# Kernel optimization log

Measured on AMD Instinct MI355X. Metric: run time of the kernel, lower is better.

Reference implementation:

```python
import jax, jax.numpy as jnp
import numpy as np

B, N, H = 256, 512, 128          # batch of subgraphs, max elements per subgraph, hidden size
NH, DEPTH = 2, 3                 # num_attention_heads (hardcoded 2 in SubGraph), depth
DH = H // NH                     # per-head dim
EPS = 1e-5
NEG = -10000.0


def setup_inputs() -> dict:
    key = jax.random.key(0)
    ks = jax.random.split(key, 12)
    s = 0.02
    x = jax.random.normal(ks[0], (B, N, H), jnp.float32)
    lengths = jax.random.randint(ks[1], (B,), 1, N + 1, jnp.int32)
    # MLP layer_0: Linear + LayerNorm + ReLU
    W0 = jax.random.normal(ks[2], (H, H), jnp.float32) * s
    b0 = jnp.zeros((H,), jnp.float32)
    g0 = jnp.ones((H,), jnp.float32)
    be0 = jnp.zeros((H,), jnp.float32)
    # MLP layer_0_again
    W1 = jax.random.normal(ks[3], (H, H), jnp.float32) * s
    b1 = jnp.zeros((H,), jnp.float32)
    g1 = jnp.ones((H,), jnp.float32)
    be1 = jnp.zeros((H,), jnp.float32)
    # GlobalGraph q/k/v per depth (no output projection in VectorNet GlobalGraph)
    Wq = jax.random.normal(ks[4], (DEPTH, H, H), jnp.float32) * s
    bq = jnp.zeros((DEPTH, H), jnp.float32)
    Wk = jax.random.normal(ks[5], (DEPTH, H, H), jnp.float32) * s
    bk = jnp.zeros((DEPTH, H), jnp.float32)
    Wv = jax.random.normal(ks[6], (DEPTH, H, H), jnp.float32) * s
    bv = jnp.zeros((DEPTH, H), jnp.float32)
    # post-block LayerNorms (layers_2)
    gl = jnp.ones((DEPTH, H), jnp.float32)
    bl = jnp.zeros((DEPTH, H), jnp.float32)
    return dict(hidden_states=x, lengths=lengths, W0=W0, b0=b0, g0=g0, be0=be0,
                W1=W1, b1=b1, g1=g1, be1=be1, Wq=Wq, bq=bq, Wk=Wk, bk=bk,
                Wv=Wv, bv=bv, gl=gl, bl=bl)


def _layer_norm(x, g, b):
    m = jnp.mean(x, axis=-1, keepdims=True)
    v = jnp.mean((x - m) ** 2, axis=-1, keepdims=True)
    return (x - m) * jax.lax.rsqrt(v + EPS) * g + b


def _mlp(x, W, b, g, be):
    return jax.nn.relu(_layer_norm(x @ W + b, g, be))


def reference(hidden_states, lengths, W0, b0, g0, be0, W1, b1, g1, be1,
              Wq, bq, Wk, bk, Wv, bv, gl, bl):
    # vectorized variable-length square mask: mask[i, :len, :len] = 1
    valid = (jnp.arange(N) < lengths[:, None])                      # [B, N] bool
    attn_mask = (valid[:, :, None] & valid[:, None, :]).astype(hidden_states.dtype)  # [B, N, N]
    bias = (1.0 - attn_mask)[:, None, :, :] * NEG                   # [B, 1, N, N]

    h = _mlp(hidden_states, W0, b0, g0, be0)
    h = _mlp(h, W1, b1, g1, be1)

    scale = 1.0 / np.sqrt(DH)
    for d in range(DEPTH):  # small fixed structural loop
        temp = h
        q = (h @ Wq[d] + bq[d]).reshape(B, N, NH, DH)
        k = (h @ Wk[d] + bk[d]).reshape(B, N, NH, DH)
        v = (h @ Wv[d] + bv[d]).reshape(B, N, NH, DH)
        scores = jnp.einsum('bnhd,bmhd->bhnm', q, k) * scale + bias  # [B, NH, N, N]
        probs = jax.nn.softmax(scores, axis=-1)
        ctx = jnp.einsum('bhnm,bmhd->bnhd', probs, v).reshape(B, N, H)
        h = _layer_norm(jax.nn.relu(ctx) + temp, gl[d], bl[d])
    return jnp.max(h, axis=1)  # [B, H]
```

## Files before the change

### kernel.cpp

```cpp
#include <hip/hip_runtime.h>
#include <hip/hip_bf16.h>

#define BB 256
#define NN 512
#define HH 128
#define MM (BB*NN)

typedef unsigned short u16;
typedef unsigned int   u32;
typedef __attribute__((ext_vector_type(8))) short bf16x8;
typedef __attribute__((ext_vector_type(4))) float f32x4;
typedef __attribute__((ext_vector_type(16))) float f32x16;

#define LOG2E  1.4426950408889634f
#define QSCALE (0.125f * LOG2E)
#define NEGB   (-10000.0f * LOG2E)

__device__ __forceinline__ int kswz(int row, int cbyte) {
  return row*128 + (cbyte ^ ((row & 7) << 4));
}
__device__ __forceinline__ int wswz(int row, int cbyte) {
  return row*256 + (cbyte ^ ((row & 7) << 4));
}

__device__ __forceinline__ u16 f2bf(float x) {
  __hip_bfloat16 h = __float2bfloat16(x);
  return *reinterpret_cast<u16*>(&h);
}
__device__ __forceinline__ float bf2f(u16 x) {
  return __uint_as_float(((u32)x) << 16);
}

__device__ __forceinline__ void gld_lds16(const void* g, void* l) {
  __builtin_amdgcn_global_load_lds(
      (__attribute__((address_space(1))) const unsigned int*)g,
      (__attribute__((address_space(3))) unsigned int*)l, 16, 0, 0);
}

__global__ __launch_bounds__(256) void wt_prep(
    const float* __restrict__ W0, const float* __restrict__ W1,
    const float* __restrict__ Wq, const float* __restrict__ Wk,
    const float* __restrict__ Wv, u16* __restrict__ wt)
{
  __shared__ u16 tile[128*128];
  const int t = threadIdx.x;
  const int i = blockIdx.x;
  const float* src;
  if (i == 0) src = W0;
  else if (i == 1) src = W1;
  else {
    const int d = (i-2)/3, which = (i-2)%3;
    src = (which==0 ? Wq : which==1 ? Wk : Wv) + d*HH*HH;
  }
  u16* dst = wt + (size_t)i*HH*HH;

  #pragma unroll
  for (int j = 0; j < 8; j++) {
    const int chunk = t + 256*j;
    const int k = chunk >> 4, c8 = (chunk & 15)*8;
    const float4 a = *(const float4*)&src[k*HH + c8];
    const float4 b = *(const float4*)&src[k*HH + c8 + 4];
    union { u16 s[8]; uint4 v; } u;
    u.s[0]=f2bf(a.x); u.s[1]=f2bf(a.y); u.s[2]=f2bf(a.z); u.s[3]=f2bf(a.w);
    u.s[4]=f2bf(b.x); u.s[5]=f2bf(b.y); u.s[6]=f2bf(b.z); u.s[7]=f2bf(b.w);
    *(uint4*)&tile[k*128 + (((chunk & 15) ^ ((k>>3)&7)) << 3)] = u.v;
  }
  __syncthreads();
  #pragma unroll
  for (int j = 0; j < 8; j++) {
    const int chunk = t + 256*j;
    const int c = chunk >> 4, kb8 = (chunk & 15)*8;
    union { u16 s[8]; uint4 v; } u;
    #pragma unroll
    for (int e = 0; e < 8; e++) {
      const int k = kb8 + e;
      u.s[e] = tile[k*128 + ((((c>>3) ^ ((k>>3)&7)) << 3) | (c & 7))];
    }
    *(uint4*)&dst[c*HH + kb8] = u.v;
  }
}

template<bool F32IN, bool LNRELU>
__device__ __forceinline__ void linear_body(
    const void* __restrict__ Xv, const u16* __restrict__ WT,
    const float* __restrict__ bias, const float* __restrict__ gamma,
    const float* __restrict__ beta, u16* __restrict__ OUT,
    u16* wt_s, u16* xs)
{
  const int t = threadIdx.x;
  const int lane = t & 63, w = t >> 6;
  const int l4 = lane >> 4, l15 = lane & 15;
  const long row0 = (long)blockIdx.x * 128;

  {
    const int rr = lane >> 4;
    const int cb = (lane & 15) * 16;
    #pragma unroll
    for (int i = 0; i < 8; i++) {
      const int seg = w*8 + i;
      const int row = seg*4 + rr;
      gld_lds16((const char*)WT + (size_t)row*256 + (cb ^ ((row & 7) << 4)),
                (char*)wt_s + seg*1024);
    }
    if constexpr (!F32IN) {
      const char* xp = (const char*)((const u16*)Xv + row0*HH);
      #pragma unroll
      for (int i = 0; i < 8; i++) {
        const int seg = w*8 + i;
        const int row = seg*4 + rr;
        gld_lds16(xp + (size_t)row*256 + (cb ^ ((row & 7) << 4)),
                  (char*)xs + seg*1024);
      }
    }
  }
  if constexpr (F32IN) {
    const float* xp = (const float*)Xv + row0*HH;
    #pragma unroll
    for (int i = 0; i < 8; i++) {
      const int chunk = t + 256*i;
      const int r = chunk >> 4, c8 = (chunk & 15)*8;
      const float4 a = *(const float4*)&xp[r*HH + c8];
      const float4 b = *(const float4*)&xp[r*HH + c8 + 4];
      union { u16 s[8]; uint4 v; } u;
      u.s[0]=f2bf(a.x); u.s[1]=f2bf(a.y); u.s[2]=f2bf(a.z); u.s[3]=f2bf(a.w);
      u.s[4]=f2bf(b.x); u.s[5]=f2bf(b.y); u.s[6]=f2bf(b.z); u.s[7]=f2bf(b.w);
      *(uint4*)((char*)xs + wswz(r, c8*2)) = u.v;
    }
  }
  __syncthreads();

  f32x4 acc[2][8];
  #pragma unroll
  for (int m = 0; m < 2; m++)
    #pragma unroll
    for (int n = 0; n < 8; n++)
      { acc[m][n][0]=0.f; acc[m][n][1]=0.f; acc[m][n][2]=0.f; acc[m][n][3]=0.f; }

  #pragma unroll
  for (int ks = 0; ks < 4; ks++) {
    bf16x8 af[2], bf[8];
    #pragma unroll
    for (int m = 0; m < 2; m++)
      af[m] = *(const bf16x8*)((const char*)xs + wswz(w*32 + m*16 + l15, ks*64 + l4*16));
    #pragma unroll
    for (int n = 0; n < 8; n++)
      bf[n] = *(const bf16x8*)((const char*)wt_s + wswz(n*16 + l15, ks*64 + l4*16));
    #pragma unroll
    for (int m = 0; m < 2; m++)
      #pragma unroll
      for (int n = 0; n < 8; n++)
        acc[m][n] = __builtin_amdgcn_mfma_f32_16x16x32_bf16(af[m], bf[n], acc[m][n], 0, 0, 0);
  }

  float bia[8], gam[8], bet[8];
  #pragma unroll
  for (int n = 0; n < 8; n++) {
    bia[n] = bias[n*16 + l15];
    if constexpr (LNRELU) { gam[n] = gamma[n*16 + l15]; bet[n] = beta[n*16 + l15]; }
  }
  #pragma unroll
  for (int m = 0; m < 2; m++) {
    #pragma unroll
    for (int r = 0; r < 4; r++) {
      const long row = row0 + w*32 + m*16 + l4*4 + r;
      float v[8];
      #pragma unroll
      for (int n = 0; n < 8; n++) v[n] = acc[m][n][r] + bia[n];
      if constexpr (LNRELU) {
        float s = 0.f, ss = 0.f;
        #pragma unroll
        for (int n = 0; n < 8; n++) { s += v[n]; ss += v[n]*v[n]; }
        #pragma unroll
        for (int off = 1; off < 16; off <<= 1) {
          s  += __shfl_xor(s,  off);
          ss += __shfl_xor(ss, off);
        }
        const float mean = s * (1.0f/128.0f);
        const float rstd = rsqrtf(ss*(1.0f/128.0f) - mean*mean + 1e-5f);
        #pragma unroll
        for (int n = 0; n < 8; n++)
          v[n] = fmaxf((v[n] - mean)*rstd*gam[n] + bet[n], 0.0f);
      }
      u16* op = OUT + row*HH + l15;
      #pragma unroll
      for (int n = 0; n < 8; n++) op[n*16] = f2bf(v[n]);
    }
  }
}

template<bool F32IN, bool LNRELU>
__global__ __launch_bounds__(256) void linear_mfma(
    const void* __restrict__ Xv, const u16* __restrict__ WT,
    const float* __restrict__ bias, const float* __restrict__ gamma,
    const float* __restrict__ beta, u16* __restrict__ OUT)
{
  __shared__ u16 wt_s[128*128];
  __shared__ u16 xs[128*128];
  linear_body<F32IN, LNRELU>(Xv, WT, bias, gamma, beta, OUT, wt_s, xs);
}

__global__ __launch_bounds__(256) void qkv_mfma(
    const u16* __restrict__ X, const u16* __restrict__ WTd,
    const float* __restrict__ bq, const float* __restrict__ bk,
    const float* __restrict__ bv,
    u16* __restrict__ qb, u16* __restrict__ kb, u16* __restrict__ vb)
{
  __shared__ u16 wt_s[128*128];
  __shared__ u16 xs[128*128];
  const int y = blockIdx.y;
  const u16* WT = WTd + y*HH*HH;
  const float* bias = (y==0) ? bq : (y==1) ? bk : bv;
  u16* OUT = (y==0) ? qb : (y==1) ? kb : vb;
  linear_body<false, false>(X, WT, bias, nullptr, nullptr, OUT, wt_s, xs);
}

__global__ __launch_bounds__(256) void transpose_v_kernel(
    const u16* __restrict__ vb, u16* __restrict__ vT)
{
  __shared__ u16 tile[128*128];
  const int t  = threadIdx.x;
  const int b  = blockIdx.x >> 2;
  const int n0 = (blockIdx.x & 3) * 128;

  #pragma unroll
  for (int i = 0; i < 8; i++) {
    const int chunk = t + 256*i;
    const int n = chunk >> 4, cslot = chunk & 15;
    uint4 d = *(const uint4*)(vb + ((size_t)(b*NN + n0 + n))*HH + cslot*8);
    *(uint4*)&tile[n*128 + ((cslot ^ ((n>>3)&7)) << 3)] = d;
  }
  __syncthreads();
  #pragma unroll
  for (int i = 0; i < 8; i++) {
    const int chunk = t + 256*i;
    const int c = chunk >> 4, nb = (chunk & 15) * 8;
    union { u16 s[8]; uint4 v; } u;
    #pragma unroll
    for (int j = 0; j < 8; j++) {
      const int n = nb + j;
      u.s[j] = tile[n*128 + ((((c>>3) ^ ((n>>3)&7)) << 3) | (c & 7))];
    }
    u16* op = vT + (((size_t)(b*2 + (c>>6)))*64 + (c & 63))*NN + n0 + nb;
    *(uint4*)op = u.v;
  }
}

__global__ __launch_bounds__(256) void attn_kernel(
    const u16* __restrict__ Q, const u16* __restrict__ K,
    const u16* __restrict__ VT, const int* __restrict__ lengths,
    u16* __restrict__ CTX)
{
  __shared__ u16 sh_q[128*64];
  __shared__ u16 sh_k[2][64*64];
  __shared__ u16 sh_v[2][64*64];
  const int t    = threadIdx.x;
  const int lane = t & 63;
  const int w    = t >> 6;
  const int bid  = blockIdx.x;
  const int qt   = bid & 3;
  const int head = (bid >> 2) & 1;
  const int b    = bid >> 3;
  const int L    = lengths[b];
  const int q0   = qt * 128;
  const int l31  = lane & 31;
  const int hi   = lane >> 5;
  const int rr8  = lane >> 3;
  const int cb8  = (lane & 7) * 16;

  const char* qbase  = (const char*)(Q + ((size_t)(b*NN + q0))*HH + head*64);
  const char* kbase0 = (const char*)(K + ((size_t)(b*NN))*HH + head*64);
  const char* vbase0 = (const char*)(VT + (((size_t)(b*2 + head))*64)*NN);

  #pragma unroll
  for (int i = 0; i < 4; i++) {
    const int seg = w*4 + i;
    const int row = seg*8 + rr8;
    gld_lds16(qbase + (size_t)row*256 + (cb8 ^ ((row&7)<<4)),
              (char*)sh_q + seg*1024);
  }
  #pragma unroll
  for (int i = 0; i < 2; i++) {
    const int seg = w*2 + i;
    const int row = seg*8 + rr8;
    const int sw = cb8 ^ ((row&7)<<4);
    gld_lds16(kbase0 + (size_t)row*256  + sw, (char*)sh_k[0] + seg*1024);
    gld_lds16(vbase0 + (size_t)row*1024 + sw, (char*)sh_v[0] + seg*1024);
  }
  __syncthreads();

  bf16x8 qf[4];
  #pragma unroll
  for (int st = 0; st < 4; st++)
    qf[st] = *(const bf16x8*)((const char*)sh_q + kswz(w*32 + l31, st*32 + hi*16));

  f32x16 cacc[2];
  #pragma unroll
  for (int r = 0; r < 16; r++) { cacc[0][r] = 0.f; cacc[1][r] = 0.f; }
  float l_run = 0.0f;

  const bool q_allv   = (q0 + w*32 + 31) < L;
  const bool q_allinv = (q0 + w*32) >= L;
  const bool qv       = (q0 + w*32 + l31) < L;
  const int  nch      = (q0 + 127 < L) ? ((L + 63) >> 6) : 8;

  for (int ch = 0; ch < nch; ch++) {
    const int cur = ch & 1;
    if (ch + 1 < nch) {
      const char* kb_ = kbase0 + (size_t)(ch+1)*64*256;
      const char* vb_ = vbase0 + (size_t)(ch+1)*128;
      #pragma unroll
      for (int i = 0; i < 2; i++) {
        const int seg = w*2 + i;
        const int row = seg*8 + rr8;
        const int sw = cb8 ^ ((row&7)<<4);
        gld_lds16(kb_ + (size_t)row*256  + sw, (char*)sh_k[cur^1] + seg*1024);
        gld_lds16(vb_ + (size_t)row*1024 + sw, (char*)sh_v[cur^1] + seg*1024);
      }
    }

    const bool skip = q_allv && (ch*64 >= L);
    if (!skip) {
      f32x16 sacc[2];
      #pragma unroll
      for (int r = 0; r < 16; r++) { sacc[0][r] = 0.f; sacc[1][r] = 0.f; }
      #pragma unroll
      for (int st = 0; st < 4; st++) {
        const bf16x8 kf0 = *(const bf16x8*)((const char*)sh_k[cur] + kswz(l31,      st*32 + hi*16));
        const bf16x8 kf1 = *(const bf16x8*)((const char*)sh_k[cur] + kswz(32 + l31, st*32 + hi*16));
        sacc[0] = __builtin_amdgcn_mfma_f32_32x32x16_bf16(kf0, qf[st], sacc[0], 0, 0, 0);
        sacc[1] = __builtin_amdgcn_mfma_f32_32x32x16_bf16(kf1, qf[st], sacc[1], 0, 0, 0);
      }

      const bool fast = (ch*64 + 63 < L) || q_allinv;
      u32 pw[2][8];
      #pragma unroll
      for (int kb2 = 0; kb2 < 2; kb2++) {
        float p[16];
        float psum = 0.f;
        if (fast) {
          #pragma unroll
          for (int r = 0; r < 16; r++) {
            p[r] = exp2f(sacc[kb2][r] * QSCALE);
            psum += p[r];
          }
        } else {
          #pragma unroll
          for (int r = 0; r < 16; r++) {
            const int key = ch*64 + kb2*32 + (r&3) + 8*(r>>2) + 4*hi;
            const float bias = (qv && key >= L) ? NEGB : 0.0f;
            p[r] = exp2f(fmaf(sacc[kb2][r], QSCALE, bias));
            psum += p[r];
          }
        }
        l_run += psum;
        #pragma unroll
        for (int mm = 0; mm < 4; mm++)
          #pragma unroll
          for (int e = 0; e < 2; e++)
            pw[kb2][mm*2+e] = (u32)f2bf(p[4*mm+2*e]) | ((u32)f2bf(p[4*mm+2*e+1]) << 16);
      }

      #pragma unroll
      for (int kb2 = 0; kb2 < 2; kb2++) {
        #pragma unroll
        for (int st = 0; st < 2; st++) {
          const u32 w00 = pw[kb2][(2*st+0)*2+0], w01 = pw[kb2][(2*st+0)*2+1];
          const u32 w10 = pw[kb2][(2*st+1)*2+0], w11 = pw[kb2][(2*st+1)*2+1];
          const u32 own0 = hi ? w10 : w00;
          const u32 own1 = hi ? w11 : w01;
          const u32 snd0 = hi ? w00 : w10;
          const u32 snd1 = hi ? w01 : w11;
          const u32 rcv0 = (u32)__shfl_xor((int)snd0, 32);
          const u32 rcv1 = (u32)__shfl_xor((int)snd1, 32);
          union { u32 u[4]; bf16x8 v; } pb;
          pb.u[0] = hi ? rcv0 : own0;
          pb.u[1] = hi ? rcv1 : own1;
          pb.u[2] = hi ? own0 : rcv0;
          pb.u[3] = hi ? own1 : rcv1;
          #pragma unroll
          for (int db = 0; db < 2; db++) {
            const bf16x8 vf = *(const bf16x8*)((const char*)sh_v[cur] +
                                kswz(db*32 + l31, kb2*64 + st*32 + hi*16));
            cacc[db] = __builtin_amdgcn_mfma_f32_32x32x16_bf16(vf, pb.v, cacc[db], 0, 0, 0);
          }
        }
      }
    }

    __syncthreads();
  }

  const float l_full = l_run + __shfl_xor(l_run, 32);
  const float inv = 1.0f / l_full;
  const int qrow = q0 + w*32 + l31;
  u16* crow = CTX + ((size_t)(b*NN) + qrow)*HH + head*64;
  #pragma unroll
  for (int db = 0; db < 2; db++)
    #pragma unroll
    for (int mm = 0; mm < 4; mm++) {
      const int dh0 = db*32 + mm*8 + hi*4;
      uint2 o;
      o.x = (u32)f2bf(cacc[db][4*mm+0]*inv) | ((u32)f2bf(cacc[db][4*mm+1]*inv) << 16);
      o.y = (u32)f2bf(cacc[db][4*mm+2]*inv) | ((u32)f2bf(cacc[db][4*mm+3]*inv) << 16);
      *(uint2*)(crow + dh0) = o;
    }
}

__global__ __launch_bounds__(256) void resln_kernel(
    const u16* __restrict__ CTX, u16* Hb,
    const float* __restrict__ gl, const float* __restrict__ bl)
{
  const int t = threadIdx.x;
  const int lane = t & 63;
  const long row = (long)blockIdx.x*4 + (t >> 6);
  const u32 craw = *(const u32*)&CTX[row*HH + lane*2];
  const u32 hraw = *(const u32*)&Hb[row*HH + lane*2];
  const float c0 = bf2f((u16)(craw & 0xffff)), c1 = bf2f((u16)(craw >> 16));
  const float h0 = bf2f((u16)(hraw & 0xffff)), h1 = bf2f((u16)(hraw >> 16));
  const float x0 = fmaxf(c0, 0.0f) + h0;
  const float x1 = fmaxf(c1, 0.0f) + h1;
  float s = x0 + x1, ss = x0*x0 + x1*x1;
  #pragma unroll
  for (int off = 1; off < 64; off <<= 1) {
    s  += __shfl_xor(s,  off);
    ss += __shfl_xor(ss, off);
  }
  const float mean = s * (1.0f/128.0f);
  const float rstd = rsqrtf(ss*(1.0f/128.0f) - mean*mean + 1e-5f);
  const float o0 = (x0 - mean)*rstd*gl[lane*2]   + bl[lane*2];
  const float o1 = (x1 - mean)*rstd*gl[lane*2+1] + bl[lane*2+1];
  *(u32*)&Hb[row*HH + lane*2] = (u32)f2bf(o0) | ((u32)f2bf(o1) << 16);
}

__global__ __launch_bounds__(256) void maxred_kernel(
    const u16* __restrict__ Hb, float* __restrict__ out)
{
  __shared__ float red[256];
  const int b = blockIdx.x;
  const int col = threadIdx.x & 127, half = threadIdx.x >> 7;
  const u16* hp = Hb + ((size_t)b*NN + half*256)*HH + col;
  float m0 = -3.0e38f, m1 = -3.0e38f, m2 = -3.0e38f, m3 = -3.0e38f;
  for (int r = 0; r < 256; r += 4) {
    m0 = fmaxf(m0, bf2f(hp[(r+0)*HH]));
    m1 = fmaxf(m1, bf2f(hp[(r+1)*HH]));
    m2 = fmaxf(m2, bf2f(hp[(r+2)*HH]));
    m3 = fmaxf(m3, bf2f(hp[(r+3)*HH]));
  }
  red[threadIdx.x] = fmaxf(fmaxf(m0, m1), fmaxf(m2, m3));
  __syncthreads();
  if (half == 0) out[(size_t)b*HH + col] = fmaxf(red[col], red[col + 128]);
}

extern "C" void kernel_launch(void* const* d_in, const int* in_sizes, int n_in,
                              void* d_out, int out_size, void* d_ws, size_t ws_size,
                              hipStream_t stream)
{
  const float* x   = (const float*)d_in[0];
  const int* lens  = (const int*)d_in[1];
  const float* W0  = (const float*)d_in[2];
  const float* b0  = (const float*)d_in[3];
  const float* g0  = (const float*)d_in[4];
  const float* be0 = (const float*)d_in[5];
  const float* W1  = (const float*)d_in[6];
  const float* b1  = (const float*)d_in[7];
  const float* g1  = (const float*)d_in[8];
  const float* be1 = (const float*)d_in[9];
  const float* Wq  = (const float*)d_in[10];
  const float* bq  = (const float*)d_in[11];
  const float* Wk  = (const float*)d_in[12];
  const float* bk  = (const float*)d_in[13];
  const float* Wv  = (const float*)d_in[14];
  const float* bv  = (const float*)d_in[15];
  const float* gl  = (const float*)d_in[16];
  const float* bl  = (const float*)d_in[17];
  float* out = (float*)d_out;

  u16* h    = (u16*)d_ws;
  u16* ctxb = h    + (size_t)MM*HH;
  u16* qb   = ctxb + (size_t)MM*HH;
  u16* kb   = qb   + (size_t)MM*HH;
  u16* vb   = kb   + (size_t)MM*HH;
  u16* vT   = vb   + (size_t)MM*HH;
  u16* wt   = vT   + (size_t)MM*HH;

  wt_prep<<<11, 256, 0, stream>>>(W0, W1, Wq, Wk, Wv, wt);

  linear_mfma<true ,true ><<<MM/128, 256, 0, stream>>>(x, wt,           b0, g0, be0, h);
  linear_mfma<false,true ><<<MM/128, 256, 0, stream>>>(h, wt + 1*HH*HH, b1, g1, be1, h);

  for (int d = 0; d < 3; d++) {
    qkv_mfma<<<dim3(MM/128, 3), 256, 0, stream>>>(
        h, wt + (2+3*d)*HH*HH, bq + d*HH, bk + d*HH, bv + d*HH, qb, kb, vb);
    transpose_v_kernel<<<BB*4, 256, 0, stream>>>(vb, vT);
    attn_kernel<<<BB*2*4, 256, 0, stream>>>(qb, kb, vT, lens, ctxb);
    resln_kernel<<<MM/4, 256, 0, stream>>>(ctxb, h, gl + d*HH, bl + d*HH);
  }
  maxred_kernel<<<BB, 256, 0, stream>>>(h, out);
}
```

Before: 578.5 us.

## Fuse QKV projections per row tile and triple-buffer attention K/V loads

```diff
diff --git a/kernel.cpp b/kernel.cpp
--- a/kernel.cpp
+++ b/kernel.cpp
@@ -81,12 +81,13 @@
 }
 
 template<bool F32IN, bool LNRELU>
-__device__ __forceinline__ void linear_body(
+__global__ __launch_bounds__(256) void linear_mfma(
     const void* __restrict__ Xv, const u16* __restrict__ WT,
     const float* __restrict__ bias, const float* __restrict__ gamma,
-    const float* __restrict__ beta, u16* __restrict__ OUT,
-    u16* wt_s, u16* xs)
-{
+    const float* __restrict__ beta, u16* __restrict__ OUT)
+{
+  __shared__ u16 wt_s[128*128];
+  __shared__ u16 xs[128*128];
   const int t = threadIdx.x;
   const int lane = t & 63, w = t >> 6;
   const int l4 = lane >> 4, l15 = lane & 15;
@@ -188,18 +189,7 @@
   }
 }
 
-template<bool F32IN, bool LNRELU>
-__global__ __launch_bounds__(256) void linear_mfma(
-    const void* __restrict__ Xv, const u16* __restrict__ WT,
-    const float* __restrict__ bias, const float* __restrict__ gamma,
-    const float* __restrict__ beta, u16* __restrict__ OUT)
-{
-  __shared__ u16 wt_s[128*128];
-  __shared__ u16 xs[128*128];
-  linear_body<F32IN, LNRELU>(Xv, WT, bias, gamma, beta, OUT, wt_s, xs);
-}
-
-__global__ __launch_bounds__(256) void qkv_mfma(
+__global__ __launch_bounds__(256) void qkv_fused(
     const u16* __restrict__ X, const u16* __restrict__ WTd,
     const float* __restrict__ bq, const float* __restrict__ bk,
     const float* __restrict__ bv,
@@ -207,11 +197,96 @@
 {
   __shared__ u16 wt_s[128*128];
   __shared__ u16 xs[128*128];
-  const int y = blockIdx.y;
-  const u16* WT = WTd + y*HH*HH;
-  const float* bias = (y==0) ? bq : (y==1) ? bk : bv;
-  u16* OUT = (y==0) ? qb : (y==1) ? kb : vb;
-  linear_body<false, false>(X, WT, bias, nullptr, nullptr, OUT, wt_s, xs);
+  const int t = threadIdx.x;
+  const int lane = t & 63, w = t >> 6;
+  const int l4 = lane >> 4, l15 = lane & 15;
+  const long row0 = (long)blockIdx.x * 128;
+  const int rr = lane >> 4;
+  const int cb = (lane & 15) * 16;
+
+  const char* xp = (const char*)(X + row0*HH);
+  #pragma unroll
+  for (int i = 0; i < 8; i++) {
+    const int seg = w*8 + i;
+    const int row = seg*4 + rr;
+    gld_lds16(xp + (size_t)row*256 + (cb ^ ((row & 7) << 4)),
+              (char*)xs + seg*1024);
+  }
+  #pragma unroll
+  for (int i = 0; i < 8; i++) {
+    const int seg = w*8 + i;
+    const int row = seg*4 + rr;
+    gld_lds16((const char*)WTd + (size_t)row*256 + (cb ^ ((row & 7) << 4)),
+              (char*)wt_s + seg*1024);
+  }
+  __syncthreads();
+
+  bf16x8 af[2][4];
+  #pragma unroll
+  for (int m = 0; m < 2; m++)
+    #pragma unroll
+    for (int ks = 0; ks < 4; ks++)
+      af[m][ks] = *(const bf16x8*)((const char*)xs + wswz(w*32 + m*16 + l15, ks*64 + l4*16));
+
+  u16* const outs[3] = {qb, kb, vb};
+  const float* const biases[3] = {bq, bk, bv};
+
+  #pragma unroll
+  for (int y = 0; y < 3; y++) {
+    f32x4 acc[2][8];
+    #pragma unroll
+    for (int m = 0; m < 2; m++)
+      #pragma unroll
+      for (int n = 0; n < 8; n++)
+        { acc[m][n][0]=0.f; acc[m][n][1]=0.f; acc[m][n][2]=0.f; acc[m][n][3]=0.f; }
+
+    #pragma unroll
+    for (int ks = 0; ks < 4; ks++) {
+      bf16x8 bf[8];
+      #pragma unroll
+      for (int n = 0; n < 8; n++)
+        bf[n] = *(const bf16x8*)((const char*)wt_s + wswz(n*16 + l15, ks*64 + l4*16));
+      #pragma unroll
+      for (int m = 0; m < 2; m++)
+        #pragma unroll
+        for (int n = 0; n < 8; n++)
+          acc[m][n] = __builtin_amdgcn_mfma_f32_16x16x32_bf16(af[m][ks], bf[n], acc[m][n], 0, 0, 0);
+    }
+    __syncthreads();
+
+    if (y < 2) {
+      const char* wp = (const char*)(WTd + (size_t)(y+1)*HH*HH);
+      #pragma unroll
+      for (int i = 0; i < 8; i++) {
+        const int seg = w*8 + i;
+        const int row = seg*4 + rr;
+        gld_lds16(wp + (size_t)row*256 + (cb ^ ((row & 7) << 4)),
+                  (char*)wt_s + seg*1024);
+      }
+      __builtin_amdgcn_sched_barrier(0);
+    }
+
+    const float* bias = biases[y];
+    u16* OUT = outs[y];
+    float bia[8];
+    #pragma unroll
+    for (int n = 0; n < 8; n++) bia[n] = bias[n*16 + l15];
+    #pragma unroll
+    for (int m = 0; m < 2; m++) {
+      #pragma unroll
+      for (int r = 0; r < 4; r++) {
+        const long row = row0 + w*32 + m*16 + l4*4 + r;
+        u16* op = OUT + row*HH + l15;
+        #pragma unroll
+        for (int n = 0; n < 8; n++) op[n*16] = f2bf(acc[m][n][r] + bia[n]);
+      }
+    }
+
+    if (y < 2) {
+      asm volatile("s_waitcnt vmcnt(0)" ::: "memory");
+      __builtin_amdgcn_s_barrier();
+    }
+  }
 }
 
 __global__ __launch_bounds__(256) void transpose_v_kernel(
@@ -251,15 +326,18 @@
     u16* __restrict__ CTX)
 {
   __shared__ u16 sh_q[128*64];
-  __shared__ u16 sh_k[2][64*64];
-  __shared__ u16 sh_v[2][64*64];
+  __shared__ u16 sh_k[3][64*64];
+  __shared__ u16 sh_v[3][64*64];
   const int t    = threadIdx.x;
   const int lane = t & 63;
   const int w    = t >> 6;
   const int bid  = blockIdx.x;
-  const int qt   = bid & 3;
-  const int head = (bid >> 2) & 1;
-  const int b    = bid >> 3;
+  const int xcd  = bid & 7;
+  const int idx  = bid >> 3;
+  const int qt   = idx & 3;
+  const int bh   = xcd + ((idx >> 2) << 3);
+  const int head = bh & 1;
+  const int b    = bh >> 1;
   const int L    = lengths[b];
   const int q0   = qt * 128;
   const int l31  = lane & 31;
@@ -271,6 +349,11 @@
   const char* kbase0 = (const char*)(K + ((size_t)(b*NN))*HH + head*64);
   const char* vbase0 = (const char*)(VT + (((size_t)(b*2 + head))*64)*NN);
 
+  const bool q_allv   = (q0 + w*32 + 31) < L;
+  const bool q_allinv = (q0 + w*32) >= L;
+  const bool qv       = (q0 + w*32 + l31) < L;
+  const int  nch      = (q0 + 127 < L) ? ((L + 63) >> 6) : 8;
+
   #pragma unroll
   for (int i = 0; i < 4; i++) {
     const int seg = w*4 + i;
@@ -286,7 +369,22 @@
     gld_lds16(kbase0 + (size_t)row*256  + sw, (char*)sh_k[0] + seg*1024);
     gld_lds16(vbase0 + (size_t)row*1024 + sw, (char*)sh_v[0] + seg*1024);
   }
-  __syncthreads();
+  if (nch > 1) {
+    const char* kb_ = kbase0 + (size_t)64*256;
+    const char* vb_ = vbase0 + (size_t)128;
+    #pragma unroll
+    for (int i = 0; i < 2; i++) {
+      const int seg = w*2 + i;
+      const int row = seg*8 + rr8;
+      const int sw = cb8 ^ ((row&7)<<4);
+      gld_lds16(kb_ + (size_t)row*256  + sw, (char*)sh_k[1] + seg*1024);
+      gld_lds16(vb_ + (size_t)row*1024 + sw, (char*)sh_v[1] + seg*1024);
+    }
+    asm volatile("s_waitcnt vmcnt(4)" ::: "memory");
+  } else {
+    asm volatile("s_waitcnt vmcnt(0)" ::: "memory");
+  }
+  __builtin_amdgcn_s_barrier();
 
   bf16x8 qf[4];
   #pragma unroll
@@ -298,24 +396,22 @@
   for (int r = 0; r < 16; r++) { cacc[0][r] = 0.f; cacc[1][r] = 0.f; }
   float l_run = 0.0f;
 
-  const bool q_allv   = (q0 + w*32 + 31) < L;
-  const bool q_allinv = (q0 + w*32) >= L;
-  const bool qv       = (q0 + w*32 + l31) < L;
-  const int  nch      = (q0 + 127 < L) ? ((L + 63) >> 6) : 8;
-
+  int cur = 0;
   for (int ch = 0; ch < nch; ch++) {
-    const int cur = ch & 1;
-    if (ch + 1 < nch) {
-      const char* kb_ = kbase0 + (size_t)(ch+1)*64*256;
-      const char* vb_ = vbase0 + (size_t)(ch+1)*128;
+    const bool more = (ch + 2 < nch);
+    if (more) {
+      const int s2 = (cur >= 1) ? cur - 1 : 2;
+      const char* kb_ = kbase0 + (size_t)(ch+2)*64*256;
+      const char* vb_ = vbase0 + (size_t)(ch+2)*128;
       #pragma unroll
       for (int i = 0; i < 2; i++) {
         const int seg = w*2 + i;
         const int row = seg*8 + rr8;
         const int sw = cb8 ^ ((row&7)<<4);
-        gld_lds16(kb_ + (size_t)row*256  + sw, (char*)sh_k[cur^1] + seg*1024);
-        gld_lds16(vb_ + (size_t)row*1024 + sw, (char*)sh_v[cur^1] + seg*1024);
-      }
+        gld_lds16(kb_ + (size_t)row*256  + sw, (char*)sh_k[s2] + seg*1024);
+        gld_lds16(vb_ + (size_t)row*1024 + sw, (char*)sh_v[s2] + seg*1024);
+      }
+      __builtin_amdgcn_sched_barrier(0);
     }
 
     const bool skip = q_allv && (ch*64 >= L);
@@ -387,7 +483,10 @@
       }
     }
 
-    __syncthreads();
+    if (more) asm volatile("s_waitcnt vmcnt(4)" ::: "memory");
+    else      asm volatile("s_waitcnt vmcnt(0)" ::: "memory");
+    __builtin_amdgcn_s_barrier();
+    cur = (cur == 2) ? 0 : cur + 1;
   }
 
   const float l_full = l_run + __shfl_xor(l_run, 32);
@@ -489,7 +588,7 @@
   linear_mfma<false,true ><<<MM/128, 256, 0, stream>>>(h, wt + 1*HH*HH, b1, g1, be1, h);
 
   for (int d = 0; d < 3; d++) {
-    qkv_mfma<<<dim3(MM/128, 3), 256, 0, stream>>>(
+    qkv_fused<<<MM/128, 256, 0, stream>>>(
         h, wt + (2+3*d)*HH*HH, bq + d*HH, bk + d*HH, bv + d*HH, qb, kb, vb);
     transpose_v_kernel<<<BB*4, 256, 0, stream>>>(vb, vT);
     attn_kernel<<<BB*2*4, 256, 0, stream>>>(qb, kb, vT, lens, ctxb);
```

New measurement: 599.7 us. +3.7%, slower.
